# Performance work log

Hardware: AMD Instinct MI355X
Metric: run time of the kernel (lower is better)

Reference implementation:

```python
import jax, jax.numpy as jnp
import numpy as np

HID, HEADS = 512, 8
C_DIM, H_DIM, W_DIM = 512, 64, 64
THETA = 100000000.0


def _angles(c, h, w, theta):
    # matches precompute_freqs_cis: angles whose polar form is freqs_cis
    n_f = c // 4
    freqs = 1.0 / theta ** (jnp.arange(0, c, 4)[:n_f].astype(jnp.float32) / c)  # (c//4,)
    th = jnp.arange(h, dtype=jnp.float32)
    tw = jnp.arange(w, dtype=jnp.float32)
    T = jnp.stack([jnp.broadcast_to(th[:, None], (h, w)),
                   jnp.broadcast_to(tw[None, :], (h, w))], axis=2)  # (h, w, 2)
    # torch cat [T*f0, T*f1, ...] along dim 2 == (h, w, c//4, 2) reshaped
    return (T[:, :, None, :] * freqs[None, None, :, None]).reshape(h, w, c // 2)


def setup_inputs() -> dict:
    key = jax.random.key(0)
    ks = jax.random.split(key, 9)
    B, S = 2, H_DIM * W_DIM
    s = 0.02
    return {
        "query": jax.random.normal(ks[0], (B, S, HID), jnp.float32),
        "key": jax.random.normal(ks[1], (B, S, HID), jnp.float32),
        "value": jax.random.normal(ks[2], (B, S, HID), jnp.float32),
        "Wq": jax.random.normal(ks[3], (HID, HID), jnp.float32) * s,
        "bq": jax.random.normal(ks[4], (HID,), jnp.float32) * s,
        "Wk": jax.random.normal(ks[5], (HID, HID), jnp.float32) * s,
        "bk": jax.random.normal(ks[6], (HID,), jnp.float32) * s,
        "Wv": jax.random.normal(ks[7], (HID, HID), jnp.float32) * s,
        "bv": jax.random.normal(ks[8], (HID,), jnp.float32) * s,
        "h": H_DIM,
        "w": W_DIM,
        "c": HID,
    }


def reference(query, key, value, Wq, bq, Wk, bk, Wv, bv, h, w, c):
    B = query.shape[0]
    hd = HID // HEADS
    ang = _angles(C_DIM, H_DIM, W_DIM, THETA)[:h, :w].reshape(h * w, c // 2)
    cos, sin = jnp.cos(ang), jnp.sin(ang)  # (S, c//2)

    Q = query @ Wq.T + bq
    K = key @ Wk.T + bk
    V = value @ Wv.T + bv

    def rot(x):  # complex multiply on consecutive pairs, in real arithmetic
        x2 = x.reshape(B, -1, c // 2, 2)
        xr, xi = x2[..., 0], x2[..., 1]
        return jnp.stack([xr * cos - xi * sin, xr * sin + xi * cos], axis=-1).reshape(B, -1, c)

    Q, K = rot(Q), rot(K)

    def heads(x):
        return x.reshape(B, -1, HEADS, hd).transpose(0, 2, 1, 3)  # (B, H, S, hd)

    Qh, Kh, Vh = heads(Q), heads(K), heads(V)
    # NOTE: original divides by head_dim (self.scale), not sqrt(head_dim)
    att = jnp.einsum('bhqd,bhkd->bhqk', Qh, Kh) / hd
    att = jax.nn.softmax(att, axis=-1)
    out = jnp.einsum('bhqk,bhkd->bhqd', att, Vh)
    return out.transpose(0, 2, 1, 3).reshape(B, -1, HID)
```

## Files before the change

### kernel.cpp

```cpp
#include <hip/hip_runtime.h>
#include <hip/hip_bf16.h>

#define S_LEN 4096
#define HDIM  64
#define NH    8

#define XFRAG_OFF 0
#define WFRAG_OFF 12582912
#define QKV_OFF   13369344
#define WS_NEED_BYTES ((size_t)(13369344 + 12582912) * 2)
#define FB_NEED_BYTES ((size_t)12582912 * 2)

typedef short s16x8 __attribute__((ext_vector_type(8)));
typedef float f32x16 __attribute__((ext_vector_type(16)));
typedef unsigned short u16x4 __attribute__((ext_vector_type(4)));

union FragU {
    s16x8 v;
    unsigned int u[4];
    unsigned short h[8];
};

static __device__ __forceinline__ unsigned int pack2_bf16(float a, float b) {
    __hip_bfloat162 h2 = __float22bfloat162_rn(float2{a, b});
    union { __hip_bfloat162 h; unsigned int u; } cv;
    cv.h = h2;
    return cv.u;
}

static __device__ __forceinline__ unsigned short to_bf16(float a) {
    __hip_bfloat16 h = __float2bfloat16(a);
    union { __hip_bfloat16 h; unsigned short u; } cv;
    cv.h = h;
    return cv.u;
}

#define Q_PRESCALE 0.022542110f
#define FREQ_L2 0.20762050593046f

__global__ __launch_bounds__(256) void conv_frag2(
    const float* __restrict__ qx, const float* __restrict__ kx,
    const float* __restrict__ vx,
    const float* __restrict__ Wq, const float* __restrict__ Wk,
    const float* __restrict__ Wv,
    unsigned short* __restrict__ xdst, unsigned short* __restrict__ wdst)
{
    const int z  = blockIdx.z;
    const int bx = blockIdx.x;
    const int tid  = threadIdx.x;
    const int wv   = tid >> 6;
    const int lane = tid & 63;
    const int row  = lane & 31;
    const int hi   = lane >> 5;

    const float* src;
    unsigned short* dst;
    if (bx < 256) {
        src = ((z == 0) ? qx : ((z == 1) ? kx : vx)) + (size_t)(bx * 32 + row) * 512 + hi * 8;
        dst = xdst + (size_t)z * 4194304 + (size_t)bx * 16384;
    } else {
        const int s = bx - 256;
        src = ((z == 0) ? Wq : ((z == 1) ? Wk : Wv)) + (size_t)(s * 32 + row) * 512 + hi * 8;
        dst = wdst + (size_t)z * 262144 + (size_t)s * 16384;
    }

    #pragma unroll
    for (int i = 0; i < 8; ++i) {
        const int kc = wv * 8 + i;
        const float4* p = (const float4*)(src + kc * 16);
        float4 x0 = p[0], x1 = p[1];
        FragU f;
        f.u[0] = pack2_bf16(x0.x, x0.y);
        f.u[1] = pack2_bf16(x0.z, x0.w);
        f.u[2] = pack2_bf16(x1.x, x1.y);
        f.u[3] = pack2_bf16(x1.z, x1.w);
        *(s16x8*)(dst + kc * 512 + lane * 8) = f.v;
    }
}

static __device__ __forceinline__ void qkv_epilogue(
    int z, const f32x16 acc[2][2], int m0, int n0, int c31, int hi,
    const float* __restrict__ bias, unsigned short* __restrict__ dst_base)
{
    if (z < 2) {
        unsigned short* dst = dst_base + (size_t)z * 4194304;
        #pragma unroll
        for (int nt = 0; nt < 2; ++nt) {
            const int s_g = n0 + nt * 32 + c31;
            const int b   = s_g >> 12;
            const int s   = s_g & 4095;
            const float pos0 = (float)(s >> 6);
            const float pos1 = (float)(s & 63);
            #pragma unroll
            for (int mt = 0; mt < 2; ++mt) {
                #pragma unroll
                for (int g = 0; g < 4; ++g) {
                    const int o_b = m0 + mt * 32 + 8 * g + 4 * hi;
                    const float4 bb = *(const float4*)(bias + o_b);
                    float v0 = acc[mt][nt][4 * g + 0] + bb.x;
                    float v1 = acc[mt][nt][4 * g + 1] + bb.y;
                    float v2 = acc[mt][nt][4 * g + 2] + bb.z;
                    float v3 = acc[mt][nt][4 * g + 3] + bb.w;
                    const float fr0 = exp2f(-(float)(o_b >> 2) * FREQ_L2);
                    float sn0, cs0, sn1, cs1;
                    __sincosf(pos0 * fr0, &sn0, &cs0);
                    __sincosf(pos1 * fr0, &sn1, &cs1);
                    float r0 = v0 * cs0 - v1 * sn0;
                    float r1 = v0 * sn0 + v1 * cs0;
                    float r2 = v2 * cs1 - v3 * sn1;
                    float r3 = v2 * sn1 + v3 * cs1;
                    if (z == 0) { r0 *= Q_PRESCALE; r1 *= Q_PRESCALE; r2 *= Q_PRESCALE; r3 *= Q_PRESCALE; }
                    const int bh = b * NH + (o_b >> 6);
                    const int k6 = o_b & 63;
                    u16x4 pk;
                    pk.x = to_bf16(r0); pk.y = to_bf16(r1);
                    pk.z = to_bf16(r2); pk.w = to_bf16(r3);
                    const size_t off = (size_t)bh * 262144 + (s >> 5) * 2048
                                     + (k6 >> 4) * 512 + (((k6 >> 3) & 1) * 32 + (s & 31)) * 8 + (k6 & 7);
                    *(u16x4*)(dst + off) = pk;
                }
            }
        }
    } else {
        unsigned short* dst = dst_base + 8388608;
        #pragma unroll
        for (int nt = 0; nt < 2; ++nt) {
            const int o  = n0 + nt * 32 + c31;
            const float bv_ = bias[o];
            const int d = o & 63, hh = o >> 6;
            #pragma unroll
            for (int mt = 0; mt < 2; ++mt) {
                #pragma unroll
                for (int g = 0; g < 4; ++g) {
                    const int s_b = m0 + mt * 32 + 8 * g + 4 * hi;
                    const int b = s_b >> 12;
                    const int s = s_b & 4095;
                    const int bh = b * NH + hh;
                    u16x4 pk;
                    pk.x = to_bf16(acc[mt][nt][4 * g + 0] + bv_);
                    pk.y = to_bf16(acc[mt][nt][4 * g + 1] + bv_);
                    pk.z = to_bf16(acc[mt][nt][4 * g + 2] + bv_);
                    pk.w = to_bf16(acc[mt][nt][4 * g + 3] + bv_);
                    const size_t off = (size_t)bh * 262144 + (s >> 5) * 2048 + (d >> 5) * 1024
                                     + ((s >> 4) & 1) * 512 + (((s >> 3) & 1) * 32 + (d & 31)) * 8 + (s & 7);
                    *(u16x4*)(dst + off) = pk;
                }
            }
        }
    }
}

__global__ __launch_bounds__(256) void qkv_gemm_rope(
    const unsigned short* __restrict__ xf, const unsigned short* __restrict__ wf,
    const float* __restrict__ bq, const float* __restrict__ bk,
    const float* __restrict__ bv, unsigned short* __restrict__ dst_base)
{
    const int z = blockIdx.z;
    const float* bias = (z == 0) ? bq : ((z == 1) ? bk : bv);
    const unsigned short* X = xf + (size_t)z * 4194304;
    const unsigned short* W = wf + (size_t)z * 262144;

    const int tid  = threadIdx.x;
    const int wv   = tid >> 6;
    const int lane = tid & 63;
    const int c31  = lane & 31;
    const int hi   = lane >> 5;
    const int wm   = wv >> 1, wn = wv & 1;

    int m0, n0;
    const unsigned short *A, *B;
    if (z < 2) {
        m0 = blockIdx.y * 128 + wm * 64;
        n0 = blockIdx.x * 128 + wn * 64;
        A = W; B = X;
    } else {
        m0 = blockIdx.x * 128 + wm * 64;
        n0 = blockIdx.y * 128 + wn * 64;
        A = X; B = W;
    }

    const unsigned short* ap0 = A + (size_t)(m0 >> 5) * 16384 + lane * 8;
    const unsigned short* ap1 = ap0 + 16384;
    const unsigned short* bp0 = B + (size_t)(n0 >> 5) * 16384 + lane * 8;
    const unsigned short* bp1 = bp0 + 16384;

    f32x16 acc[2][2];
    #pragma unroll
    for (int a = 0; a < 2; ++a)
    #pragma unroll
    for (int b = 0; b < 2; ++b)
    #pragma unroll
    for (int r = 0; r < 16; ++r) acc[a][b][r] = 0.f;

    #pragma unroll 4
    for (int kc = 0; kc < 32; ++kc) {
        const int ko = kc * 512;
        s16x8 a0 = *(const s16x8*)(ap0 + ko);
        s16x8 a1 = *(const s16x8*)(ap1 + ko);
        s16x8 b0 = *(const s16x8*)(bp0 + ko);
        s16x8 b1 = *(const s16x8*)(bp1 + ko);
        acc[0][0] = __builtin_amdgcn_mfma_f32_32x32x16_bf16(a0, b0, acc[0][0], 0, 0, 0);
        acc[0][1] = __builtin_amdgcn_mfma_f32_32x32x16_bf16(a0, b1, acc[0][1], 0, 0, 0);
        acc[1][0] = __builtin_amdgcn_mfma_f32_32x32x16_bf16(a1, b0, acc[1][0], 0, 0, 0);
        acc[1][1] = __builtin_amdgcn_mfma_f32_32x32x16_bf16(a1, b1, acc[1][1], 0, 0, 0);
    }

    qkv_epilogue(z, acc, m0, n0, c31, hi, bias, dst_base);
}

__global__ __launch_bounds__(256) void qkv_rope_f32(
    const float* __restrict__ q_in, const float* __restrict__ k_in,
    const float* __restrict__ v_in,
    const float* __restrict__ Wq, const float* __restrict__ bq,
    const float* __restrict__ Wk, const float* __restrict__ bk,
    const float* __restrict__ Wv, const float* __restrict__ bv,
    unsigned short* __restrict__ dst_base)
{
    const int z = blockIdx.z;
    const float* Xr = (z == 0) ? q_in : ((z == 1) ? k_in : v_in);
    const float* Wr = (z == 0) ? Wq   : ((z == 1) ? Wk   : Wv);
    const float* bias = (z == 0) ? bq : ((z == 1) ? bk : bv);

    const int tid  = threadIdx.x;
    const int wv   = tid >> 6;
    const int lane = tid & 63;
    const int c31  = lane & 31;
    const int hi   = lane >> 5;
    const int wm   = wv >> 1, wn = wv & 1;

    int m0, n0;
    const float *A, *B;
    if (z < 2) { m0 = blockIdx.y * 128 + wm * 64; n0 = blockIdx.x * 128 + wn * 64; A = Wr; B = Xr; }
    else       { m0 = blockIdx.x * 128 + wm * 64; n0 = blockIdx.y * 128 + wn * 64; A = Xr; B = Wr; }

    f32x16 acc[2][2];
    #pragma unroll
    for (int a = 0; a < 2; ++a)
    #pragma unroll
    for (int b = 0; b < 2; ++b)
    #pragma unroll
    for (int r = 0; r < 16; ++r) acc[a][b][r] = 0.f;

    for (int kc = 0; kc < 32; ++kc) {
        const int kofs = kc * 16 + hi * 8;
        FragU a_f[2], b_f[2];
        #pragma unroll
        for (int mt = 0; mt < 2; ++mt) {
            const float4* p = (const float4*)(A + (size_t)(m0 + mt * 32 + c31) * 512 + kofs);
            float4 x0 = p[0], x1 = p[1];
            a_f[mt].u[0] = pack2_bf16(x0.x, x0.y);
            a_f[mt].u[1] = pack2_bf16(x0.z, x0.w);
            a_f[mt].u[2] = pack2_bf16(x1.x, x1.y);
            a_f[mt].u[3] = pack2_bf16(x1.z, x1.w);
        }
        #pragma unroll
        for (int nt = 0; nt < 2; ++nt) {
            const float4* p = (const float4*)(B + (size_t)(n0 + nt * 32 + c31) * 512 + kofs);
            float4 x0 = p[0], x1 = p[1];
            b_f[nt].u[0] = pack2_bf16(x0.x, x0.y);
            b_f[nt].u[1] = pack2_bf16(x0.z, x0.w);
            b_f[nt].u[2] = pack2_bf16(x1.x, x1.y);
            b_f[nt].u[3] = pack2_bf16(x1.z, x1.w);
        }
        #pragma unroll
        for (int mt = 0; mt < 2; ++mt)
        #pragma unroll
        for (int nt = 0; nt < 2; ++nt)
            acc[mt][nt] = __builtin_amdgcn_mfma_f32_32x32x16_bf16(
                a_f[mt].v, b_f[nt].v, acc[mt][nt], 0, 0, 0);
    }

    qkv_epilogue(z, acc, m0, n0, c31, hi, bias, dst_base);
}

__global__ __launch_bounds__(256, 4) void flash_attn_st(
    const unsigned short* __restrict__ qkv, float* __restrict__ out)
{
    __shared__ __align__(16) unsigned char smem[8192 + 16384 + 256];
    unsigned short* sQ = (unsigned short*)smem;
    float* sOb = (float*)(smem + 8192);
    float* sL  = (float*)(smem + 8192 + 16384);

    const int tid  = threadIdx.x;
    const int wv   = tid >> 6;
    const int lane = tid & 63;
    const int c31  = lane & 31;
    const int hi   = lane >> 5;
    const int qs   = wv >> 1;
    const int ks   = wv & 1;
    const int q0   = blockIdx.x * 64;
    const int bh   = blockIdx.y;

    const unsigned short* Qb  = qkv + (size_t)bh * 262144;
    const unsigned short* Kb  = qkv + (size_t)4194304 + (size_t)bh * 262144;
    const unsigned short* Vtb = qkv + (size_t)8388608 + (size_t)bh * 262144;

    #pragma unroll
    for (int i = 0; i < 2; ++i) {
        const int idx   = tid + i * 256;
        const int chunk = idx >> 6;
        const int ln    = idx & 63;
        *(s16x8*)(sQ + chunk * 512 + ln * 8) =
            *(const s16x8*)(Qb + (size_t)((q0 >> 5) + (chunk >> 2)) * 2048 + (chunk & 3) * 512 + ln * 8);
    }
    __syncthreads();

    const unsigned short* sQw = sQ + qs * 2048 + lane * 8;

    f32x16 o_acc[2];
    #pragma unroll
    for (int dt = 0; dt < 2; ++dt)
    #pragma unroll
    for (int r = 0; r < 16; ++r) o_acc[dt][r] = 0.f;
    float l_acc = 0.f;

    const unsigned short* kp = Kb  + (size_t)ks * 2048 + lane * 8;
    const unsigned short* vp = Vtb + (size_t)ks * 2048 + lane * 8;

    s16x8 ka[4];
    #pragma unroll
    for (int kc = 0; kc < 4; ++kc)
        ka[kc] = *(const s16x8*)(kp + kc * 512);

    for (int it = 0; it < 64; ++it) {
        s16x8 va[2][2];
        va[0][0] = *(const s16x8*)(vp);
        va[0][1] = *(const s16x8*)(vp + 512);
        va[1][0] = *(const s16x8*)(vp + 1024);
        va[1][1] = *(const s16x8*)(vp + 1536);
        vp += 4096;

        f32x16 st;
        #pragma unroll
        for (int r = 0; r < 16; ++r) st[r] = 0.f;
        #pragma unroll
        for (int kc = 0; kc < 4; ++kc) {
            s16x8 qf = *(const s16x8*)(sQw + kc * 512);
            st = __builtin_amdgcn_mfma_f32_32x32x16_bf16(ka[kc], qf, st, 0, 0, 0);
        }

        kp += 4096;
        if (it < 63) {
            #pragma unroll
            for (int kc = 0; kc < 4; ++kc)
                ka[kc] = *(const s16x8*)(kp + kc * 512);
        }

        unsigned int up[8];
        {
            float ls0 = 0.f, ls1 = 0.f;
            #pragma unroll
            for (int qq = 0; qq < 8; ++qq) {
                float p0 = __builtin_amdgcn_exp2f(st[2 * qq]);
                float p1 = __builtin_amdgcn_exp2f(st[2 * qq + 1]);
                ls0 += p0; ls1 += p1;
                up[qq] = pack2_bf16(p0, p1);
            }
            l_acc += ls0 + ls1;
        }

        #pragma unroll
        for (int k2 = 0; k2 < 2; ++k2) {
            const unsigned int a0 = up[4 * k2 + 0];
            const unsigned int a1 = up[4 * k2 + 1];
            const unsigned int a2 = up[4 * k2 + 2];
            const unsigned int a3 = up[4 * k2 + 3];
            const unsigned int s0 = (unsigned int)__shfl_xor((int)(hi ? a0 : a2), 32);
            const unsigned int s1 = (unsigned int)__shfl_xor((int)(hi ? a1 : a3), 32);
            FragU pb;
            pb.u[0] = hi ? s0 : a0;
            pb.u[1] = hi ? s1 : a1;
            pb.u[2] = hi ? a2 : s0;
            pb.u[3] = hi ? a3 : s1;
            #pragma unroll
            for (int dt = 0; dt < 2; ++dt)
                o_acc[dt] = __builtin_amdgcn_mfma_f32_32x32x16_bf16(
                    va[dt][k2], pb.v, o_acc[dt], 0, 0, 0);
        }
    }

    const float lw = l_acc + __shfl_xor(l_acc, 32);
    if (ks == 1) {
        if (lane < 32) sL[qs * 32 + lane] = lw;
        #pragma unroll
        for (int dt = 0; dt < 2; ++dt)
        #pragma unroll
        for (int r = 0; r < 16; ++r) {
            const int d = dt * 32 + (r & 3) + 8 * (r >> 2) + 4 * hi;
            sOb[qs * 2048 + d * 32 + c31] = o_acc[dt][r];
        }
    }
    __syncthreads();
    if (ks == 0) {
        #pragma unroll
        for (int dt = 0; dt < 2; ++dt)
        #pragma unroll
        for (int r = 0; r < 16; ++r) {
            const int d = dt * 32 + (r & 3) + 8 * (r >> 2) + 4 * hi;
            o_acc[dt][r] += sOb[qs * 2048 + d * 32 + c31];
        }
        const float rinv = 1.f / (lw + sL[qs * 32 + c31]);
        const int b  = bh >> 3;
        const int hh = bh & 7;
        const int s  = q0 + qs * 32 + c31;
        float* orow = out + ((size_t)b * S_LEN + s) * 512 + hh * 64;
        #pragma unroll
        for (int dt = 0; dt < 2; ++dt) {
            #pragma unroll
            for (int g = 0; g < 4; ++g) {
                float4 vv;
                vv.x = o_acc[dt][4 * g + 0] * rinv;
                vv.y = o_acc[dt][4 * g + 1] * rinv;
                vv.z = o_acc[dt][4 * g + 2] * rinv;
                vv.w = o_acc[dt][4 * g + 3] * rinv;
                *(float4*)(orow + dt * 32 + 8 * g + 4 * hi) = vv;
            }
        }
    }
}

extern "C" void kernel_launch(void* const* d_in, const int* in_sizes, int n_in,
                              void* d_out, int out_size, void* d_ws, size_t ws_size,
                              hipStream_t stream) {
    (void)in_sizes; (void)n_in; (void)out_size;
    const float* q_in = (const float*)d_in[0];
    const float* k_in = (const float*)d_in[1];
    const float* v_in = (const float*)d_in[2];
    const float* Wq   = (const float*)d_in[3];
    const float* bq   = (const float*)d_in[4];
    const float* Wk   = (const float*)d_in[5];
    const float* bk   = (const float*)d_in[6];
    const float* Wv   = (const float*)d_in[7];
    const float* bv   = (const float*)d_in[8];
    unsigned short* ws = (unsigned short*)d_ws;
    float* out = (float*)d_out;

    if (ws_size >= WS_NEED_BYTES) {
        conv_frag2<<<dim3(272, 1, 3), 256, 0, stream>>>(
            q_in, k_in, v_in, Wq, Wk, Wv, ws + XFRAG_OFF, ws + WFRAG_OFF);
        qkv_gemm_rope<<<dim3(64, 4, 3), 256, 0, stream>>>(
            ws + XFRAG_OFF, ws + WFRAG_OFF, bq, bk, bv, ws + QKV_OFF);
        flash_attn_st<<<dim3(64, 16), 256, 0, stream>>>(ws + QKV_OFF, out);
    } else {
        qkv_rope_f32<<<dim3(64, 4, 3), 256, 0, stream>>>(
            q_in, k_in, v_in, Wq, bq, Wk, bk, Wv, bv, ws);
        flash_attn_st<<<dim3(64, 16), 256, 0, stream>>>(ws, out);
    }
}
```

Before: 236.1 us.

## Coalesce fp32->bf16 fragment conversion via LDS; compute softmax row sums with MFMA

```diff
diff --git a/kernel.cpp b/kernel.cpp
--- a/kernel.cpp
+++ b/kernel.cpp
@@ -9,7 +9,6 @@
 #define WFRAG_OFF 12582912
 #define QKV_OFF   13369344
 #define WS_NEED_BYTES ((size_t)(13369344 + 12582912) * 2)
-#define FB_NEED_BYTES ((size_t)12582912 * 2)
 
 typedef short s16x8 __attribute__((ext_vector_type(8)));
 typedef float f32x16 __attribute__((ext_vector_type(16)));
@@ -38,43 +37,51 @@
 #define Q_PRESCALE 0.022542110f
 #define FREQ_L2 0.20762050593046f
 
-__global__ __launch_bounds__(256) void conv_frag2(
+__global__ __launch_bounds__(256) void conv_frag3(
     const float* __restrict__ qx, const float* __restrict__ kx,
     const float* __restrict__ vx,
     const float* __restrict__ Wq, const float* __restrict__ Wk,
     const float* __restrict__ Wv,
     unsigned short* __restrict__ xdst, unsigned short* __restrict__ wdst)
 {
+    __shared__ __align__(16) unsigned short slds[16640];
+
     const int z  = blockIdx.z;
     const int bx = blockIdx.x;
     const int tid  = threadIdx.x;
-    const int wv   = tid >> 6;
+    const int w    = tid >> 6;
     const int lane = tid & 63;
-    const int row  = lane & 31;
-    const int hi   = lane >> 5;
 
     const float* src;
     unsigned short* dst;
     if (bx < 256) {
-        src = ((z == 0) ? qx : ((z == 1) ? kx : vx)) + (size_t)(bx * 32 + row) * 512 + hi * 8;
+        src = ((z == 0) ? qx : ((z == 1) ? kx : vx)) + (size_t)bx * 32 * 512;
         dst = xdst + (size_t)z * 4194304 + (size_t)bx * 16384;
     } else {
         const int s = bx - 256;
-        src = ((z == 0) ? Wq : ((z == 1) ? Wk : Wv)) + (size_t)(s * 32 + row) * 512 + hi * 8;
+        src = ((z == 0) ? Wq : ((z == 1) ? Wk : Wv)) + (size_t)s * 32 * 512;
         dst = wdst + (size_t)z * 262144 + (size_t)s * 16384;
     }
 
     #pragma unroll
     for (int i = 0; i < 8; ++i) {
-        const int kc = wv * 8 + i;
-        const float4* p = (const float4*)(src + kc * 16);
+        const int r = w * 8 + i;
+        const float4* p = (const float4*)(src + (size_t)r * 512 + lane * 8);
         float4 x0 = p[0], x1 = p[1];
         FragU f;
         f.u[0] = pack2_bf16(x0.x, x0.y);
         f.u[1] = pack2_bf16(x0.z, x0.w);
         f.u[2] = pack2_bf16(x1.x, x1.y);
         f.u[3] = pack2_bf16(x1.z, x1.w);
-        *(s16x8*)(dst + kc * 512 + lane * 8) = f.v;
+        *(s16x8*)(slds + (lane >> 1) * 520 + ((lane & 1) * 32 + r) * 8) = f.v;
+    }
+    __syncthreads();
+
+    #pragma unroll
+    for (int i = 0; i < 8; ++i) {
+        const int kc = w * 8 + i;
+        s16x8 v = *(const s16x8*)(slds + kc * 520 + lane * 8);
+        *(s16x8*)(dst + kc * 512 + lane * 8) = v;
     }
 }
 
@@ -307,12 +314,18 @@
 
     const unsigned short* sQw = sQ + qs * 2048 + lane * 8;
 
+    FragU ones;
+    ones.u[0] = 0x3F803F80u; ones.u[1] = 0x3F803F80u;
+    ones.u[2] = 0x3F803F80u; ones.u[3] = 0x3F803F80u;
+
     f32x16 o_acc[2];
+    f32x16 l_frag;
     #pragma unroll
     for (int dt = 0; dt < 2; ++dt)
     #pragma unroll
     for (int r = 0; r < 16; ++r) o_acc[dt][r] = 0.f;
-    float l_acc = 0.f;
+    #pragma unroll
+    for (int r = 0; r < 16; ++r) l_frag[r] = 0.f;
 
     const unsigned short* kp = Kb  + (size_t)ks * 2048 + lane * 8;
     const unsigned short* vp = Vtb + (size_t)ks * 2048 + lane * 8;
@@ -347,16 +360,11 @@
         }
 
         unsigned int up[8];
-        {
-            float ls0 = 0.f, ls1 = 0.f;
-            #pragma unroll
-            for (int qq = 0; qq < 8; ++qq) {
-                float p0 = __builtin_amdgcn_exp2f(st[2 * qq]);
-                float p1 = __builtin_amdgcn_exp2f(st[2 * qq + 1]);
-                ls0 += p0; ls1 += p1;
-                up[qq] = pack2_bf16(p0, p1);
-            }
-            l_acc += ls0 + ls1;
+        #pragma unroll
+        for (int qq = 0; qq < 8; ++qq) {
+            const float p0 = __builtin_amdgcn_exp2f(st[2 * qq]);
+            const float p1 = __builtin_amdgcn_exp2f(st[2 * qq + 1]);
+            up[qq] = (__float_as_uint(p1) & 0xFFFF0000u) | (__float_as_uint(p0) >> 16);
         }
 
         #pragma unroll
@@ -376,10 +384,11 @@
             for (int dt = 0; dt < 2; ++dt)
                 o_acc[dt] = __builtin_amdgcn_mfma_f32_32x32x16_bf16(
                     va[dt][k2], pb.v, o_acc[dt], 0, 0, 0);
-        }
-    }
-
-    const float lw = l_acc + __shfl_xor(l_acc, 32);
+            l_frag = __builtin_amdgcn_mfma_f32_32x32x16_bf16(ones.v, pb.v, l_frag, 0, 0, 0);
+        }
+    }
+
+    const float lw = l_frag[0];
     if (ks == 1) {
         if (lane < 32) sL[qs * 32 + lane] = lw;
         #pragma unroll
@@ -436,7 +445,7 @@
     float* out = (float*)d_out;
 
     if (ws_size >= WS_NEED_BYTES) {
-        conv_frag2<<<dim3(272, 1, 3), 256, 0, stream>>>(
+        conv_frag3<<<dim3(272, 1, 3), 256, 0, stream>>>(
             q_in, k_in, v_in, Wq, Wk, Wv, ws + XFRAG_OFF, ws + WFRAG_OFF);
         qkv_gemm_rope<<<dim3(64, 4, 3), 256, 0, stream>>>(
             ws + XFRAG_OFF, ws + WFRAG_OFF, bq, bk, bv, ws + QKV_OFF);
```

Result: no change. 234.4 us (-0.7%).
